# Kernel tuning notes

Measured on AMD Instinct MI355X. Metric: run time of the kernel, lower is better.

The kernel has to match this reference:

```python
import jax, jax.numpy as jnp
import numpy as np

EPS = 1e-5

def _conv3x3(x, w):
    # x: [N,C,H,W], w: [O,I,3,3], stride 1, padding 1
    return jax.lax.conv_general_dilated(
        x, w, window_strides=(1, 1), padding=((1, 1), (1, 1)),
        dimension_numbers=('NCHW', 'OIHW', 'NCHW'))

def _bn(x, gamma, beta, rmean, rvar):
    # inference-mode BatchNorm2d over channel dim
    scale = gamma * jax.lax.rsqrt(rvar + EPS)
    return x * scale[None, :, None, None] + (beta - rmean * scale)[None, :, None, None]

def setup_inputs() -> dict:
    key = jax.random.key(0)
    ks = jax.random.split(key, 8)
    N, C, H, W = 32, 256, 56, 56
    x = jax.random.normal(ks[0], (N, C, H, W), dtype=jnp.float32)
    w1 = jax.random.normal(ks[1], (C, C, 3, 3), dtype=jnp.float32) * 0.05
    w2 = jax.random.normal(ks[2], (C, C, 3, 3), dtype=jnp.float32) * 0.05
    g1 = jax.random.normal(ks[3], (C,), dtype=jnp.float32) * 0.1 + 1.0
    b1 = jax.random.normal(ks[4], (C,), dtype=jnp.float32) * 0.1
    g2 = jax.random.normal(ks[5], (C,), dtype=jnp.float32) * 0.1 + 1.0
    b2 = jax.random.normal(ks[6], (C,), dtype=jnp.float32) * 0.1
    rm1 = jax.random.normal(jax.random.fold_in(key, 10), (C,), dtype=jnp.float32) * 0.1
    rv1 = jax.random.uniform(jax.random.fold_in(key, 11), (C,), dtype=jnp.float32) + 0.5
    rm2 = jax.random.normal(jax.random.fold_in(key, 12), (C,), dtype=jnp.float32) * 0.1
    rv2 = jax.random.uniform(jax.random.fold_in(key, 13), (C,), dtype=jnp.float32) + 0.5
    return {'x': x, 'w1': w1, 'g1': g1, 'b1': b1, 'rm1': rm1, 'rv1': rv1,
            'w2': w2, 'g2': g2, 'b2': b2, 'rm2': rm2, 'rv2': rv2}

def reference(x, w1, g1, b1, rm1, rv1, w2, g2, b2, rm2, rv2):
    identity = x
    out = jax.nn.relu(_bn(_conv3x3(x, w1), g1, b1, rm1, rv1))
    out = _bn(_conv3x3(out, w2), g2, b2, rm2, rv2)
    return jax.nn.relu(out + identity)
```

## Files before the change

### kernel.cpp

```cpp
#include <hip/hip_runtime.h>
#include <hip/hip_bf16.h>

#define NN 32
#define CC 256
#define HH 56
#define WW 56
#define HP 58
#define PIX (HH * WW)
#define MTOT (NN * PIX)
#define BN_EPS 1e-5f

using f32x4  = __attribute__((ext_vector_type(4))) float;
using short8 = __attribute__((ext_vector_type(8))) short;

__device__ __forceinline__ void gload16(const void* g, void* l) {
    __builtin_amdgcn_global_load_lds(
        (const __attribute__((address_space(1))) void*)g,
        (__attribute__((address_space(3))) void*)l, 16, 0, 0);
}


__global__ __launch_bounds__(256) void transform_x(const float* __restrict__ x,
                                                   __hip_bfloat16* __restrict__ xt) {
    __shared__ float t[64][65];
    const int tx = threadIdx.x & 63, ty = threadIdx.x >> 6;
    const int c0 = blockIdx.x * 64, h = blockIdx.y, n = blockIdx.z;
    #pragma unroll
    for (int i = 0; i < 16; ++i) {
        const int c = ty + i * 4;
        float v = 0.f;
        if (tx < WW) v = x[(((size_t)n * CC + c0 + c) * HH + h) * WW + tx];
        t[c][tx] = v;
    }
    __syncthreads();
    #pragma unroll
    for (int i = 0; i < 16; ++i) {
        const int w = ty + i * 4;
        if (w < WW)
            xt[((n * HP + h + 1) * HP + (w + 1)) * CC + c0 + tx] = __float2bfloat16(t[tx][w]);
    }
}

__global__ void transform_w(const float* __restrict__ w, __hip_bfloat16* __restrict__ wt) {
    const int co = blockIdx.x, tap = blockIdx.y, ci = threadIdx.x;
    wt[(tap * CC + co) * CC + ci] = __float2bfloat16(w[(co * CC + ci) * 9 + tap]);
}

__global__ void zero_borders(__hip_bfloat16* __restrict__ buf) {
    const int i = blockIdx.x, n = blockIdx.y;
    int h, w;
    if (i < 58)       { h = 0;              w = i; }
    else if (i < 116) { h = 57;             w = i - 58; }
    else if (i < 172) { h = 1 + (i - 116);  w = 0; }
    else              { h = 1 + (i - 172);  w = 57; }
    buf[((n * HP + h) * HP + w) * CC + threadIdx.x] = __float2bfloat16(0.f);
}

template<bool SECOND>
__global__ __launch_bounds__(512, 2) void conv_mfma(
    const __hip_bfloat16* __restrict__ act,
    const __hip_bfloat16* __restrict__ wt,
    const float* __restrict__ g, const float* __restrict__ bb,
    const float* __restrict__ rm, const float* __restrict__ rv,
    const float* __restrict__ identity,
    void* __restrict__ out)
{
    __shared__ short S[2][2][256][64];
    char* SB = (char*)S;

    const int tid  = threadIdx.x;
    const int lane = tid & 63;
    const int wid  = tid >> 6;
    const int wm   = wid >> 2;
    const int wn   = wid & 3;

    const int bid = blockIdx.x;
    const int mb  = (bid & 7) * 49 + (bid >> 3);

    const int scol = (lane & 7) ^ (lane >> 3);

    int abase[2][2], bbase[2][2];
    #pragma unroll
    for (int h2 = 0; h2 < 2; ++h2)
        #pragma unroll
        for (int j = 0; j < 2; ++j) {
            const int r = h2 * 128 + j * 64 + wid * 8 + (lane >> 3);
            const int p = mb * 256 + r;
            const int n   = p / PIX;
            const int rem = p - n * PIX;
            const int h = rem / WW, w = rem - h * WW;
            abase[h2][j] = (((n * HP + h) * HP + w) * CC + scol * 8) * 2;
            bbase[h2][j] = (r * CC + scol * 8) * 2;
        }

    f32x4 acc[8][4];
    #pragma unroll
    for (int i = 0; i < 8; ++i)
        #pragma unroll
        for (int j = 0; j < 4; ++j)
            acc[i][j] = (f32x4){0.f, 0.f, 0.f, 0.f};

    const char* actB = (const char*)act;
    const char* wtB  = (const char*)wt;

    auto stageA = [&](int buf, int h2, int t) {
        const int cic = t / 9, tap = t - cic * 9;
        const int dh = tap / 3, dw = tap - dh * 3;
        const int aoff = (dh * HP + dw) * (CC * 2) + cic * 128;
        char* dst = SB + buf * 65536 + h2 * 16384 + wid * 1024;
        gload16(actB + abase[h2][0] + aoff, dst);
        gload16(actB + abase[h2][1] + aoff, dst + 8192);
    };
    auto stageB = [&](int buf, int h2, int t) {
        const int cic = t / 9, tap = t - cic * 9;
        const int boff = tap * (CC * CC * 2) + cic * 128;
        char* dst = SB + buf * 65536 + 32768 + h2 * 16384 + wid * 1024;
        gload16(wtB + bbase[h2][0] + boff, dst);
        gload16(wtB + bbase[h2][1] + boff, dst + 8192);
    };

    const int rlane = lane & 15;
    const int xorb  = (rlane & 7) << 4;
    const int colb  = (lane >> 4) << 4;

    stageA(0, 0, 0); stageA(0, 1, 0); stageB(0, 0, 0); stageB(0, 1, 0);

    short8 bfr[2][4];

    #pragma unroll 1
    for (int t = 0; t < 36; ++t) {
        const int cur = t & 1;
        const bool last = (t == 35);
        const char* Ab = SB + cur * 65536;
        const char* Bb = SB + cur * 65536 + 32768;
        #pragma unroll
        for (int p = 0; p < 4; ++p) {
            if (!last) {
                if      (p == 0) stageA(cur ^ 1, 0, t + 1);
                else if (p == 1) stageA(cur ^ 1, 1, t + 1);
                else if (p == 2) stageB(cur ^ 1, 0, t + 1);
                else             stageB(cur ^ 1, 1, t + 1);
            }
            if (p == 0) {
                if (!last) asm volatile("s_waitcnt vmcnt(2)" ::: "memory");
                else       asm volatile("s_waitcnt vmcnt(0)" ::: "memory");
                __builtin_amdgcn_s_barrier();
                __builtin_amdgcn_sched_barrier(0);
            }
            const int coladdr = ((p & 1) * 64 + colb) ^ xorb;
            short8 afr[4];
            #pragma unroll
            for (int mi = 0; mi < 4; ++mi)
                afr[mi] = *(const short8*)(Ab
                    + (wm * 128 + ((p >> 1) * 4 + mi) * 16 + rlane) * 128 + coladdr);
            if (p < 2) {
                #pragma unroll
                for (int nf = 0; nf < 4; ++nf)
                    bfr[p][nf] = *(const short8*)(Bb
                        + (wn * 64 + nf * 16 + rlane) * 128 + coladdr);
            }
            if (p != 0) {
                __builtin_amdgcn_sched_barrier(0);
                __builtin_amdgcn_s_barrier();
                __builtin_amdgcn_sched_barrier(0);
            }
            __builtin_amdgcn_s_setprio(1);
            #pragma unroll
            for (int mi = 0; mi < 4; ++mi)
                #pragma unroll
                for (int nf = 0; nf < 4; ++nf)
                    acc[(p >> 1) * 4 + mi][nf] = __builtin_amdgcn_mfma_f32_16x16x32_bf16(
                        afr[mi], bfr[p & 1][nf], acc[(p >> 1) * 4 + mi][nf], 0, 0, 0);
            __builtin_amdgcn_s_setprio(0);
            __builtin_amdgcn_sched_barrier(0);
            __builtin_amdgcn_s_barrier();
            __builtin_amdgcn_sched_barrier(0);
        }
    }

    const int lm = lane >> 4, ln = lane & 15;
    #pragma unroll
    for (int nf = 0; nf < 4; ++nf) {
        const int co = wn * 64 + nf * 16 + ln;
        const float scale = g[co] * rsqrtf(rv[co] + BN_EPS);
        const float bias  = bb[co] - rm[co] * scale;
        #pragma unroll
        for (int mf = 0; mf < 8; ++mf) {
            const int p0  = mb * 256 + wm * 128 + mf * 16 + lm * 4;
            const int n   = p0 / PIX;
            const int pr  = p0 - n * PIX;
            f32x4 v = acc[mf][nf];
            if (SECOND) {
                const size_t off = (size_t)(n * CC + co) * PIX + pr;
                const float4 id = *(const float4*)(identity + off);
                float4 o;
                o.x = fmaxf(fmaf(v[0], scale, bias) + id.x, 0.f);
                o.y = fmaxf(fmaf(v[1], scale, bias) + id.y, 0.f);
                o.z = fmaxf(fmaf(v[2], scale, bias) + id.z, 0.f);
                o.w = fmaxf(fmaf(v[3], scale, bias) + id.w, 0.f);
                *(float4*)((float*)out + off) = o;
            } else {
                const int h = pr / WW, w = pr - h * WW;
                __hip_bfloat16* yp = (__hip_bfloat16*)out
                    + ((n * HP + h + 1) * HP + (w + 1)) * CC + co;
                #pragma unroll
                for (int r = 0; r < 4; ++r)
                    yp[r * CC] = __float2bfloat16(fmaxf(fmaf(v[r], scale, bias), 0.f));
            }
        }
    }
}

__device__ __forceinline__ float rb_(float v) { return __bfloat162float(__float2bfloat16(v)); }

template<bool SECOND>
__global__ __launch_bounds__(256) void conv_bn_naive(
    const void* __restrict__ in_v, const float* __restrict__ wmat,
    const float* __restrict__ g, const float* __restrict__ b,
    const float* __restrict__ rm, const float* __restrict__ rv,
    const float* __restrict__ identity, void* __restrict__ out_v)
{
    constexpr int CI_CHUNK = 8;
    __shared__ float xs[CI_CHUNK][3][58];
    __shared__ float ws_s[4][CI_CHUNK][9];
    const int tid = threadIdx.x;
    const int co_l = tid >> 6;
    const int wl_raw = tid & 63;
    const int wl = wl_raw < (WW - 1) ? wl_raw : (WW - 1);
    const int co = blockIdx.x * 4 + co_l;
    const int h = blockIdx.y, n = blockIdx.z;
    const float* in_f = (const float*)in_v;
    const __hip_bfloat16* in_b = (const __hip_bfloat16*)in_v;
    float acc = 0.f;
    for (int ci0 = 0; ci0 < CC; ci0 += CI_CHUNK) {
        __syncthreads();
        for (int i = tid; i < CI_CHUNK * 3 * 58; i += 256) {
            int ci = i / 174, rem = i - ci * 174, r = rem / 58, col = rem - r * 58;
            int h_in = h + r - 1, x_col = col - 1;
            float v = 0.f;
            if ((unsigned)h_in < HH && (unsigned)x_col < WW) {
                int idx = ((n * CC + ci0 + ci) * HH + h_in) * WW + x_col;
                v = SECOND ? __bfloat162float(in_b[idx]) : rb_(in_f[idx]);
            }
            xs[ci][r][col] = v;
        }
        for (int i = tid; i < 4 * CI_CHUNK * 9; i += 256) {
            int c_l = i / (CI_CHUNK * 9), rem = i - c_l * (CI_CHUNK * 9);
            int ci = rem / 9, k = rem - ci * 9;
            ws_s[c_l][ci][k] = rb_(wmat[(blockIdx.x * 4 + c_l) * CC * 9 + (ci0 + ci) * 9 + k]);
        }
        __syncthreads();
        #pragma unroll
        for (int ci = 0; ci < CI_CHUNK; ++ci) {
            float wr[9];
            #pragma unroll
            for (int k = 0; k < 9; ++k) wr[k] = ws_s[co_l][ci][k];
            #pragma unroll
            for (int dh = 0; dh < 3; ++dh)
                #pragma unroll
                for (int dw = 0; dw < 3; ++dw)
                    acc += xs[ci][dh][wl + dw] * wr[dh * 3 + dw];
        }
    }
    if (wl_raw < WW) {
        float scale = g[co] * rsqrtf(rv[co] + BN_EPS);
        float bias = b[co] - rm[co] * scale;
        float v = acc * scale + bias;
        int oidx = ((n * CC + co) * HH + h) * WW + wl_raw;
        if (SECOND) {
            v += identity[oidx];
            ((float*)out_v)[oidx] = fmaxf(v, 0.f);
        } else {
            ((__hip_bfloat16*)out_v)[oidx] = __float2bfloat16(fmaxf(v, 0.f));
        }
    }
}

extern "C" void kernel_launch(void* const* d_in, const int* in_sizes, int n_in,
                              void* d_out, int out_size, void* d_ws, size_t ws_size,
                              hipStream_t stream) {
    const float* x   = (const float*)d_in[0];
    const float* w1  = (const float*)d_in[1];
    const float* g1  = (const float*)d_in[2];
    const float* b1  = (const float*)d_in[3];
    const float* rm1 = (const float*)d_in[4];
    const float* rv1 = (const float*)d_in[5];
    const float* w2  = (const float*)d_in[6];
    const float* g2  = (const float*)d_in[7];
    const float* b2  = (const float*)d_in[8];
    const float* rm2 = (const float*)d_in[9];
    const float* rv2 = (const float*)d_in[10];

    const size_t XT_B = (size_t)NN * HP * HP * CC * 2;
    const size_t WT_B = (size_t)9 * CC * CC * 2;
    const size_t NEED = 2 * XT_B + 2 * WT_B;

    if (ws_size < NEED) {
        __hip_bfloat16* tmp = (__hip_bfloat16*)d_ws;
        dim3 grid(CC / 4, HH, NN);
        conv_bn_naive<false><<<grid, 256, 0, stream>>>(x, w1, g1, b1, rm1, rv1, nullptr, tmp);
        conv_bn_naive<true ><<<grid, 256, 0, stream>>>(tmp, w2, g2, b2, rm2, rv2, x, d_out);
        return;
    }

    char* ws = (char*)d_ws;
    __hip_bfloat16* xt  = (__hip_bfloat16*)ws;
    __hip_bfloat16* y1  = (__hip_bfloat16*)(ws + XT_B);
    __hip_bfloat16* wt1 = (__hip_bfloat16*)(ws + 2 * XT_B);
    __hip_bfloat16* wt2 = (__hip_bfloat16*)(ws + 2 * XT_B + WT_B);

    zero_borders<<<dim3(228, NN), 256, 0, stream>>>(xt);
    zero_borders<<<dim3(228, NN), 256, 0, stream>>>(y1);
    transform_x <<<dim3(4, HH, NN), 256, 0, stream>>>(x, xt);
    transform_w <<<dim3(CC, 9), 256, 0, stream>>>(w1, wt1);
    transform_w <<<dim3(CC, 9), 256, 0, stream>>>(w2, wt2);

    conv_mfma<false><<<392, 512, 0, stream>>>(xt, wt1, g1, b1, rm1, rv1, nullptr, y1);
    conv_mfma<true ><<<392, 512, 0, stream>>>(y1, wt2, g2, b2, rm2, rv2, x, d_out);
}
```

Before: 353.1 us.

## Issue whole next-tile prefetch at once and cut barriers to two per k-step

Replaces the four-phase interleaved schedule with a simpler one. Each iteration now issues all eight global-to-LDS loads for the next tile up front, waits for the current tile, and keeps only one barrier before and one after the compute. The old code had barriers and sched_barriers between every sub-phase. This removes per-phase synchronisation overhead and lets the compiler schedule LDS reads and MFMAs freely. The cost is losing the fine-grained interleaving of global loads with MFMA work, and the compiler may reorder instructions less favourably.

```diff
diff --git a/kernel.cpp b/kernel.cpp
--- a/kernel.cpp
+++ b/kernel.cpp
@@ -103,67 +103,57 @@
     const char* actB = (const char*)act;
     const char* wtB  = (const char*)wt;
 
-    auto stageA = [&](int buf, int h2, int t) {
+    auto stageTile = [&](int buf, int t) {
         const int cic = t / 9, tap = t - cic * 9;
         const int dh = tap / 3, dw = tap - dh * 3;
         const int aoff = (dh * HP + dw) * (CC * 2) + cic * 128;
-        char* dst = SB + buf * 65536 + h2 * 16384 + wid * 1024;
-        gload16(actB + abase[h2][0] + aoff, dst);
-        gload16(actB + abase[h2][1] + aoff, dst + 8192);
-    };
-    auto stageB = [&](int buf, int h2, int t) {
-        const int cic = t / 9, tap = t - cic * 9;
         const int boff = tap * (CC * CC * 2) + cic * 128;
-        char* dst = SB + buf * 65536 + 32768 + h2 * 16384 + wid * 1024;
-        gload16(wtB + bbase[h2][0] + boff, dst);
-        gload16(wtB + bbase[h2][1] + boff, dst + 8192);
+        char* da = SB + buf * 65536 + wid * 1024;
+        char* db = SB + buf * 65536 + 32768 + wid * 1024;
+        #pragma unroll
+        for (int h2 = 0; h2 < 2; ++h2) {
+            gload16(actB + abase[h2][0] + aoff, da + h2 * 16384);
+            gload16(actB + abase[h2][1] + aoff, da + h2 * 16384 + 8192);
+            gload16(wtB  + bbase[h2][0] + boff, db + h2 * 16384);
+            gload16(wtB  + bbase[h2][1] + boff, db + h2 * 16384 + 8192);
+        }
     };
 
     const int rlane = lane & 15;
     const int xorb  = (rlane & 7) << 4;
     const int colb  = (lane >> 4) << 4;
 
-    stageA(0, 0, 0); stageA(0, 1, 0); stageB(0, 0, 0); stageB(0, 1, 0);
-
-    short8 bfr[2][4];
+    stageTile(0, 0);
 
     #pragma unroll 1
     for (int t = 0; t < 36; ++t) {
         const int cur = t & 1;
-        const bool last = (t == 35);
+        if (t < 35) {
+            stageTile(cur ^ 1, t + 1);
+            asm volatile("s_waitcnt vmcnt(8)" ::: "memory");
+        } else {
+            asm volatile("s_waitcnt vmcnt(0)" ::: "memory");
+        }
+        __builtin_amdgcn_s_barrier();
+        asm volatile("" ::: "memory");
+
         const char* Ab = SB + cur * 65536;
         const char* Bb = SB + cur * 65536 + 32768;
+        short8 bfr[2][4];
         #pragma unroll
         for (int p = 0; p < 4; ++p) {
-            if (!last) {
-                if      (p == 0) stageA(cur ^ 1, 0, t + 1);
-                else if (p == 1) stageA(cur ^ 1, 1, t + 1);
-                else if (p == 2) stageB(cur ^ 1, 0, t + 1);
-                else             stageB(cur ^ 1, 1, t + 1);
-            }
-            if (p == 0) {
-                if (!last) asm volatile("s_waitcnt vmcnt(2)" ::: "memory");
-                else       asm volatile("s_waitcnt vmcnt(0)" ::: "memory");
-                __builtin_amdgcn_s_barrier();
-                __builtin_amdgcn_sched_barrier(0);
-            }
             const int coladdr = ((p & 1) * 64 + colb) ^ xorb;
-            short8 afr[4];
-            #pragma unroll
-            for (int mi = 0; mi < 4; ++mi)
-                afr[mi] = *(const short8*)(Ab
-                    + (wm * 128 + ((p >> 1) * 4 + mi) * 16 + rlane) * 128 + coladdr);
             if (p < 2) {
                 #pragma unroll
                 for (int nf = 0; nf < 4; ++nf)
                     bfr[p][nf] = *(const short8*)(Bb
                         + (wn * 64 + nf * 16 + rlane) * 128 + coladdr);
             }
-            if (p != 0) {
-                __builtin_amdgcn_sched_barrier(0);
-                __builtin_amdgcn_s_barrier();
-                __builtin_amdgcn_sched_barrier(0);
-            }
+            short8 afr[4];
+            #pragma unroll
+            for (int mi = 0; mi < 4; ++mi)
+                afr[mi] = *(const short8*)(Ab
+                    + (wm * 128 + ((p >> 1) * 4 + mi) * 16 + rlane) * 128 + coladdr);
             __builtin_amdgcn_s_setprio(1);
             #pragma unroll
             for (int mi = 0; mi < 4; ++mi)
@@ -172,10 +162,10 @@
                     acc[(p >> 1) * 4 + mi][nf] = __builtin_amdgcn_mfma_f32_16x16x32_bf16(
                         afr[mi], bfr[p & 1][nf], acc[(p >> 1) * 4 + mi][nf], 0, 0, 0);
             __builtin_amdgcn_s_setprio(0);
-            __builtin_amdgcn_sched_barrier(0);
-            __builtin_amdgcn_s_barrier();
-            __builtin_amdgcn_sched_barrier(0);
-        }
+        }
+        asm volatile("" ::: "memory");
+        __builtin_amdgcn_s_barrier();
+        asm volatile("" ::: "memory");
     }
 
     const int lm = lane >> 4, ln = lane & 15;
```

Result: faster. 344.6 us (-2.4%).

## Prefetch B two stages ahead and fold border zeroing into transform_x

Applied to the files above, without the earlier changes.

The conv main loop is restructured so weight (B) tiles are prefetched two k-steps ahead into the current buffer after its B fragments are consumed, while A tiles stay one step ahead. The single wait/barrier at the start of each k-step is replaced by a wait at the last phase and barriers in every phase. sched_barrier calls become plain compiler memory fences. Separately, transform_x now writes the padded borders of xt itself, which removes one zero_borders launch. The new schedule depends on exact vmcnt accounting, and loosening the scheduling fences could let the compiler reorder instructions.

```diff
diff --git a/kernel.cpp b/kernel.cpp
--- a/kernel.cpp
+++ b/kernel.cpp
@@ -25,19 +25,25 @@
     __shared__ float t[64][65];
     const int tx = threadIdx.x & 63, ty = threadIdx.x >> 6;
     const int c0 = blockIdx.x * 64, h = blockIdx.y, n = blockIdx.z;
-    #pragma unroll
-    for (int i = 0; i < 16; ++i) {
-        const int c = ty + i * 4;
-        float v = 0.f;
-        if (tx < WW) v = x[(((size_t)n * CC + c0 + c) * HH + h) * WW + tx];
-        t[c][tx] = v;
+    const bool hIn = (h >= 1) && (h <= HH);
+    if (hIn) {
+        #pragma unroll
+        for (int i = 0; i < 16; ++i) {
+            const int c = ty + i * 4;
+            float v = 0.f;
+            if (tx < WW) v = x[(((size_t)n * CC + c0 + c) * HH + (h - 1)) * WW + tx];
+            t[c][tx] = v;
+        }
     }
     __syncthreads();
     #pragma unroll
     for (int i = 0; i < 16; ++i) {
-        const int w = ty + i * 4;
-        if (w < WW)
-            xt[((n * HP + h + 1) * HP + (w + 1)) * CC + c0 + tx] = __float2bfloat16(t[tx][w]);
+        const int w0 = ty + i * 4;
+        if (w0 < HP) {
+            float v = 0.f;
+            if (hIn && w0 >= 1 && w0 <= WW) v = t[tx][w0 - 1];
+            xt[((n * HP + h) * HP + w0) * CC + c0 + tx] = __float2bfloat16(v);
+        }
     }
 }
 
@@ -123,30 +129,24 @@
     const int xorb  = (rlane & 7) << 4;
     const int colb  = (lane >> 4) << 4;
 
-    stageA(0, 0, 0); stageA(0, 1, 0); stageB(0, 0, 0); stageB(0, 1, 0);
+    stageB(0, 0, 0); stageB(0, 1, 0); stageA(0, 0, 0); stageA(0, 1, 0);
+    stageB(1, 0, 1); stageB(1, 1, 1);
+    asm volatile("s_waitcnt vmcnt(4)" ::: "memory");
+    __builtin_amdgcn_s_barrier();
+    asm volatile("" ::: "memory");
 
     short8 bfr[2][4];
-
     #pragma unroll 1
     for (int t = 0; t < 36; ++t) {
         const int cur = t & 1;
-        const bool last = (t == 35);
         const char* Ab = SB + cur * 65536;
         const char* Bb = SB + cur * 65536 + 32768;
         #pragma unroll
         for (int p = 0; p < 4; ++p) {
-            if (!last) {
-                if      (p == 0) stageA(cur ^ 1, 0, t + 1);
-                else if (p == 1) stageA(cur ^ 1, 1, t + 1);
-                else if (p == 2) stageB(cur ^ 1, 0, t + 1);
-                else             stageB(cur ^ 1, 1, t + 1);
-            }
-            if (p == 0) {
-                if (!last) asm volatile("s_waitcnt vmcnt(2)" ::: "memory");
-                else       asm volatile("s_waitcnt vmcnt(0)" ::: "memory");
-                __builtin_amdgcn_s_barrier();
-                __builtin_amdgcn_sched_barrier(0);
-            }
+            if (p == 0)      { if (t < 35) stageA(cur ^ 1, 0, t + 1); }
+            else if (p == 1) { if (t < 35) stageA(cur ^ 1, 1, t + 1); }
+            else if (p == 2) { if (t < 34) stageB(cur,     0, t + 2); }
+            else             { if (t < 34) stageB(cur,     1, t + 2); }
             const int coladdr = ((p & 1) * 64 + colb) ^ xorb;
             short8 afr[4];
             #pragma unroll
@@ -159,11 +159,13 @@
                     bfr[p][nf] = *(const short8*)(Bb
                         + (wn * 64 + nf * 16 + rlane) * 128 + coladdr);
             }
-            if (p != 0) {
-                __builtin_amdgcn_sched_barrier(0);
-                __builtin_amdgcn_s_barrier();
-                __builtin_amdgcn_sched_barrier(0);
+            if (p == 3) {
+                if (t <= 33)      asm volatile("s_waitcnt vmcnt(4)" ::: "memory");
+                else if (t == 34) asm volatile("s_waitcnt vmcnt(0)" ::: "memory");
             }
+            asm volatile("" ::: "memory");
+            __builtin_amdgcn_s_barrier();
+            asm volatile("" ::: "memory");
             __builtin_amdgcn_s_setprio(1);
             #pragma unroll
             for (int mi = 0; mi < 4; ++mi)
@@ -172,9 +174,9 @@
                     acc[(p >> 1) * 4 + mi][nf] = __builtin_amdgcn_mfma_f32_16x16x32_bf16(
                         afr[mi], bfr[p & 1][nf], acc[(p >> 1) * 4 + mi][nf], 0, 0, 0);
             __builtin_amdgcn_s_setprio(0);
-            __builtin_amdgcn_sched_barrier(0);
+            asm volatile("" ::: "memory");
             __builtin_amdgcn_s_barrier();
-            __builtin_amdgcn_sched_barrier(0);
+            asm volatile("" ::: "memory");
         }
     }
 
@@ -309,9 +311,8 @@
     __hip_bfloat16* wt1 = (__hip_bfloat16*)(ws + 2 * XT_B);
     __hip_bfloat16* wt2 = (__hip_bfloat16*)(ws + 2 * XT_B + WT_B);
 
-    zero_borders<<<dim3(228, NN), 256, 0, stream>>>(xt);
     zero_borders<<<dim3(228, NN), 256, 0, stream>>>(y1);
-    transform_x <<<dim3(4, HH, NN), 256, 0, stream>>>(x, xt);
+    transform_x <<<dim3(4, HP, NN), 256, 0, stream>>>(x, xt);
     transform_w <<<dim3(CC, 9), 256, 0, stream>>>(w1, wt1);
     transform_w <<<dim3(CC, 9), 256, 0, stream>>>(w2, wt2);
 
```

Result: faster. 337.2 us (-4.5%).
